# Performance work log

Hardware: AMD Instinct MI355X
Metric: run time of the kernel (lower is better)

## Reference

```python
import jax, jax.numpy as jnp
import numpy as np

N_NODES = 100000
N_EDGES = 2000000
FEAT = 4
H = 64
L = 3  # num_mp_layers
E = 2  # edge_types


def _p(key, shape, scale=0.05):
    return jax.random.normal(key, shape, dtype=jnp.float32) * scale


def setup_inputs() -> dict:
    key = jax.random.key(0)
    ks = jax.random.split(key, 24)
    inp = {
        "x": jax.random.normal(ks[0], (N_NODES, FEAT), dtype=jnp.float32),
        "node_type": jax.random.randint(ks[1], (N_NODES,), 0, 3),
        "edge_index": jax.random.randint(ks[2], (2, N_EDGES), 0, N_NODES),
        "edge_type": jax.random.randint(ks[3], (N_EDGES,), 0, E),
        # input_proj: Linear(4,64) + LayerNorm(64)
        "in_w": _p(ks[4], (FEAT, H)), "in_b": _p(ks[5], (H,)),
        "ln_g": jnp.ones((H,), jnp.float32), "ln_b": jnp.zeros((H,), jnp.float32),
        # per-layer, per-edge-type message MLPs: Linear(2H,H) -> ReLU -> Linear(H,H)
        "mlp_w1": _p(ks[6], (L, E, 2 * H, H)), "mlp_b1": _p(ks[7], (L, E, H)),
        "mlp_w2": _p(ks[8], (L, E, H, H)), "mlp_b2": _p(ks[9], (L, E, H)),
        # per-layer GRUCell(H,H): gates ordered [r, z, n] as in torch
        "gru_wi": _p(ks[10], (L, H, 3 * H)), "gru_wh": _p(ks[11], (L, H, 3 * H)),
        "gru_bi": _p(ks[12], (L, 3 * H)), "gru_bh": _p(ks[13], (L, 3 * H)),
        # readout: Linear(H,H) -> ReLU -> Linear(H,1)
        "ro_w1": _p(ks[14], (H, H)), "ro_b1": _p(ks[15], (H,)),
        "ro_w2": _p(ks[16], (H, 1)), "ro_b2": _p(ks[17], (1,)),
    }
    return inp


def _layernorm(h, g, b, eps=1e-5):
    mu = jnp.mean(h, axis=-1, keepdims=True)
    var = jnp.mean(jnp.square(h - mu), axis=-1, keepdims=True)
    return (h - mu) * jax.lax.rsqrt(var + eps) * g + b


def _forward(x, edge_index, edge_type, node_type,
             in_w, in_b, ln_g, ln_b,
             mlp_w1, mlp_b1, mlp_w2, mlp_b2,
             gru_wi, gru_wh, gru_bi, gru_bh,
             ro_w1, ro_b1, ro_w2, ro_b2):
    n = x.shape[0]
    # input projection (dropout is identity at inference)
    h = jax.nn.relu(_layernorm(x @ in_w + in_b, ln_g, ln_b))
    src, dst = edge_index[0], edge_index[1]
    for l in range(L):
        # gather -> concat: (M, 2H)
        mi = jnp.concatenate([h[src], h[dst]], axis=1)
        msg = jnp.zeros((mi.shape[0], H), dtype=h.dtype)
        for e in range(E):
            m = jax.nn.relu(mi @ mlp_w1[l, e] + mlp_b1[l, e]) @ mlp_w2[l, e] + mlp_b2[l, e]
            msg = msg + jnp.where((edge_type == e)[:, None], m, jnp.zeros((), h.dtype))
        # scatter_add over destination nodes
        agg = jax.ops.segment_sum(msg, dst, num_segments=n)
        # GRUCell(agg, h), torch gate order [r, z, n]
        gi = agg @ gru_wi[l] + gru_bi[l]
        gh = h @ gru_wh[l] + gru_bh[l]
        i_r, i_z, i_n = jnp.split(gi, 3, axis=-1)
        h_r, h_z, h_n = jnp.split(gh, 3, axis=-1)
        r = jax.nn.sigmoid(i_r + h_r)
        z = jax.nn.sigmoid(i_z + h_z)
        nn_ = jnp.tanh(i_n + r * h_n)
        h = (1.0 - z) * nn_ + z * h
    out = jax.nn.relu(h @ ro_w1 + ro_b1) @ ro_w2 + ro_b2  # (N, 1)
    # additive correction for data qubits (node_type==0); other nodes zeroed
    corr = jnp.where(node_type == 0, x[:, 0] + out[:, 0], jnp.zeros((), x.dtype))
    return corr


def reference(x, node_type, edge_index, edge_type,
              in_w, in_b, ln_g, ln_b,
              mlp_w1, mlp_b1, mlp_w2, mlp_b2,
              gru_wi, gru_wh, gru_bi, gru_bh,
              ro_w1, ro_b1, ro_w2, ro_b2):
    return _forward(x, edge_index, edge_type, node_type,
                    in_w, in_b, ln_g, ln_b,
                    mlp_w1, mlp_b1, mlp_w2, mlp_b2,
                    gru_wi, gru_wh, gru_bi, gru_bh,
                    ro_w1, ro_b1, ro_w2, ro_b2)
```

## Files before the change

kernel.cpp:

```cpp
#include <hip/hip_runtime.h>

typedef unsigned int u32;
typedef unsigned short u16;
typedef unsigned long long u64;

using short8 = __attribute__((ext_vector_type(8))) short;
using f32x4  = __attribute__((ext_vector_type(4))) float;

__device__ __forceinline__ u32 f2bf(float f) {
    u32 u = __float_as_uint(f);
    return (u + 0x7fffu + ((u >> 16) & 1u)) >> 16;
}
__device__ __forceinline__ u32 pk(float a, float b) {
    return f2bf(a) | (f2bf(b) << 16);
}
__device__ __forceinline__ u32 f2bf_fast(float f) {
    return (__float_as_uint(f) + 0x8000u) >> 16;
}
__device__ __forceinline__ u32 pk_fast(float a, float b) {
    return f2bf_fast(a) | (f2bf_fast(b) << 16);
}
__device__ __forceinline__ float bflo(u32 u) { return __uint_as_float(u << 16); }
__device__ __forceinline__ float bfhi(u32 u) { return __uint_as_float(u & 0xffff0000u); }
__device__ __forceinline__ float bfu(u16 u) { return __uint_as_float(((u32)u) << 16); }

union U8 { u32 u[4]; short8 v; };

__global__ void k_input_proj(const float* __restrict__ x, const float* __restrict__ in_w,
                             const float* __restrict__ in_b, const float* __restrict__ ln_g,
                             const float* __restrict__ ln_b, u16* __restrict__ hbf, int n_nodes) {
    const int lane = threadIdx.x & 63;
    const int node = blockIdx.x * 4 + (threadIdx.x >> 6);
    if (node >= n_nodes) return;
    float acc = in_b[lane];
#pragma unroll
    for (int k = 0; k < 4; ++k) acc = fmaf(x[node * 4 + k], in_w[k * 64 + lane], acc);
    float s = acc;
#pragma unroll
    for (int off = 32; off > 0; off >>= 1) s += __shfl_xor(s, off);
    float mu = s * (1.f / 64.f);
    float d = acc - mu;
    float vs = d * d;
#pragma unroll
    for (int off = 32; off > 0; off >>= 1) vs += __shfl_xor(vs, off);
    float inv = rsqrtf(vs * (1.f / 64.f) + 1e-5f);
    float hv = fmaxf(d * inv * ln_g[lane] + ln_b[lane], 0.f);
    hbf[(size_t)node * 64 + lane] = (u16)f2bf(hv);
}

__global__ void k_hist(const int* __restrict__ dst, const int* __restrict__ ety,
                       int* __restrict__ cnt, int M, int N) {
    int i = blockIdx.x * 256 + threadIdx.x;
    if (i < M) atomicAdd(&cnt[(ety[i] & 1) * N + dst[i]], 1);
}

__global__ void k_scan1(int* __restrict__ data, int* __restrict__ part, int N) {
    __shared__ int s[1024];
    const int t = threadIdx.x;
    const int i = blockIdx.x * 1024 + t;
    int v = (i < N) ? data[i] : 0;
    s[t] = v;
    __syncthreads();
#pragma unroll
    for (int d = 1; d < 1024; d <<= 1) {
        int x = (t >= d) ? s[t - d] : 0;
        __syncthreads();
        s[t] += x;
        __syncthreads();
    }
    if (i < N) data[i] = s[t] - v;
    if (t == 1023) part[blockIdx.x] = s[1023];
}

__global__ void k_scan2(int* __restrict__ part, int nb) {
    const int l = threadIdx.x & 63;
    int base = 0;
    for (int s = 0; s < nb; s += 64) {
        int i = s + l;
        int orig = (i < nb) ? part[i] : 0;
        int x = orig;
#pragma unroll
        for (int off = 1; off < 64; off <<= 1) {
            int t = __shfl_up(x, off);
            if (l >= off) x += t;
        }
        if (i < nb) part[i] = base + x - orig;
        base += __shfl(x, 63);
    }
}

__global__ void k_scan3(int* __restrict__ data, const int* __restrict__ part, int N,
                        int saveIdx, int* __restrict__ slot) {
    int i = blockIdx.x * 1024 + threadIdx.x;
    if (i < N) {
        int v = data[i] + part[blockIdx.x];
        data[i] = v;
        if (i == saveIdx) slot[0] = v;
    }
}

__global__ void k_filldst(const int* __restrict__ off, int* __restrict__ dstP,
                          int NB, int N, int M) {
    int b = blockIdx.x * 256 + threadIdx.x;
    if (b >= NB) return;
    int s = off[b];
    int e = (b + 1 < NB) ? off[b + 1] : M;
    int d = (b >= N) ? b - N : b;
    for (int p = s; p < e; ++p) dstP[p] = d;
}

__global__ void k_scatter(const int* __restrict__ src, const int* __restrict__ dst,
                          const int* __restrict__ ety, int* __restrict__ cursor,
                          int* __restrict__ srcP, int M, int N, int nd8) {
    const int g = blockIdx.x & 7;
    const int nb = gridDim.x >> 3;
    const int bi = blockIdx.x >> 3;
    for (int e = bi * 256 + threadIdx.x; e < M; e += nb * 256) {
        int d = dst[e];
        if (d / nd8 == g) {
            int t = ety[e] & 1;
            int pos = atomicAdd(&cursor[t * N + d], 1);
            srcP[pos] = src[e] & 0x3FFFFFFF;
        }
    }
}

__global__ __launch_bounds__(256, 2) void k_edge_mlp(
    const u16* __restrict__ hbf, const int* __restrict__ srcP, const int* __restrict__ dstP,
    const int* __restrict__ t0p, const float* __restrict__ w1, const float* __restrict__ b1,
    const float* __restrict__ w2, const float* __restrict__ b2,
    float* __restrict__ agg, int M) {
    __shared__ u16 sHid[4][4608];
    __shared__ u16 sMsg[4][4864];

    const int tid = threadIdx.x;
    const int l = tid & 63, wv = tid >> 6;
    const int l15 = l & 15, quad = l >> 4;
    const f32x4 vz = {0.f, 0.f, 0.f, 0.f};

    const int T0 = *t0p;
    const int half = gridDim.x >> 1;
    const int ty = (blockIdx.x >= half) ? 1 : 0;
    const int bi = ty ? (int)blockIdx.x - half : (int)blockIdx.x;

    const int n_tiles = (M + 63) >> 6;
    const int tlo = ty ? (T0 >> 6) : 0;
    const int thi = ty ? n_tiles : ((T0 + 63) >> 6);
    const int lo = ty ? T0 : 0;
    const int hi = ty ? M : T0;
    const int range = thi - tlo;
    const int per = (range + half - 1) / half;
    const int c0 = tlo + bi * per;
    const int c1 = min(c0 + per, thi);

    short8 Bf1[4][4], Bf2[2][4];
    float b1r[4], b2r[4];
#pragma unroll
    for (int ni = 0; ni < 4; ++ni) {
        const int c = ni * 16 + l15;
        b1r[ni] = b1[ty * 64 + c];
        b2r[ni] = b2[ty * 64 + c];
#pragma unroll
        for (int s = 0; s < 4; ++s) {
            U8 tmp;
            const float* wp = w1 + (size_t)ty * 8192 + (size_t)(s * 32 + quad * 8) * 64 + c;
#pragma unroll
            for (int jp = 0; jp < 4; ++jp) tmp.u[jp] = pk(wp[(2 * jp) * 64], wp[(2 * jp + 1) * 64]);
            Bf1[s][ni] = tmp.v;
        }
#pragma unroll
        for (int s = 0; s < 2; ++s) {
            U8 tmp;
            const float* wp = w2 + (size_t)ty * 4096 + (size_t)(s * 32 + quad * 8) * 64 + c;
#pragma unroll
            for (int jp = 0; jp < 4; ++jp) tmp.u[jp] = pk(wp[(2 * jp) * 64], wp[(2 * jp + 1) * 64]);
            Bf2[s][ni] = tmp.v;
        }
    }

    u16* hid = sHid[wv];
    u16* msg = sMsg[wv];

    int t = c0 + wv;
    int mdr_c = -1;
    int rs[4], rd[4];
    short8 a1[4][4];
    if (t < c1) {
        int ec = min((t << 6) + l, M - 1);
        int ms = srcP[ec];
        mdr_c = dstP[ec];
#pragma unroll
        for (int mi = 0; mi < 4; ++mi) {
            rs[mi] = __shfl(ms, mi * 16 + l15);
            rd[mi] = __shfl(mdr_c, mi * 16 + l15);
        }
#pragma unroll
        for (int mi = 0; mi < 4; ++mi)
#pragma unroll
            for (int s = 0; s < 4; ++s) {
                const int row = (s < 2) ? rs[mi] : rd[mi];
                a1[mi][s] = *(const short8*)(hbf + (size_t)row * 64 + (s & 1) * 32 + quad * 8);
            }
    }

    for (; t < c1; t += 4) {
        const int base = t << 6;
        const int ecn = min(((t + 4) << 6) + l, M - 1);
        int msr_n = srcP[ecn];
        int mdr_n = dstP[ecn];

#pragma unroll
        for (int mi = 0; mi < 4; ++mi) {
            f32x4 acc[4] = {vz, vz, vz, vz};
#pragma unroll
            for (int s = 0; s < 4; ++s)
#pragma unroll
                for (int ni = 0; ni < 4; ++ni)
                    acc[ni] = __builtin_amdgcn_mfma_f32_16x16x32_bf16(a1[mi][s], Bf1[s][ni], acc[ni], 0, 0, 0);
#pragma unroll
            for (int ni = 0; ni < 4; ++ni) {
                const int c = ni * 16 + l15;
#pragma unroll
                for (int r = 0; r < 4; ++r) {
                    float hv = fmaxf(acc[ni][r] + b1r[ni], 0.f);
                    hid[(mi * 16 + quad * 4 + r) * 72 + c] = (u16)f2bf_fast(hv);
                }
            }
        }

#pragma unroll
        for (int mi = 0; mi < 4; ++mi) {
            rs[mi] = __shfl(msr_n, mi * 16 + l15);
            rd[mi] = __shfl(mdr_n, mi * 16 + l15);
        }
#pragma unroll
        for (int mi = 0; mi < 4; ++mi)
#pragma unroll
            for (int s = 0; s < 4; ++s) {
                const int row = (s < 2) ? rs[mi] : rd[mi];
                a1[mi][s] = *(const short8*)(hbf + (size_t)row * 64 + (s & 1) * 32 + quad * 8);
            }

#pragma unroll
        for (int mi = 0; mi < 4; ++mi) {
            short8 a2a = *(const short8*)(hid + (mi * 16 + l15) * 72 + quad * 8);
            short8 a2b = *(const short8*)(hid + (mi * 16 + l15) * 72 + 32 + quad * 8);
#pragma unroll
            for (int ni = 0; ni < 4; ++ni) {
                f32x4 tt = __builtin_amdgcn_mfma_f32_16x16x32_bf16(a2a, Bf2[0][ni], vz, 0, 0, 0);
                f32x4 m2 = __builtin_amdgcn_mfma_f32_16x16x32_bf16(a2b, Bf2[1][ni], tt, 0, 0, 0);
                const int c = ni * 16 + l15;
                const int e0 = mi * 16 + quad * 4;
                const float bb = b2r[ni];
                *(u32*)(msg + c * 76 + e0) = pk_fast(m2[0] + bb, m2[1] + bb);
                *(u32*)(msg + c * 76 + e0 + 2) = pk_fast(m2[2] + bb, m2[3] + bb);
            }
        }

        {
            int eg = base + l;
            int dvz = (eg >= lo && eg < hi) ? mdr_c : -1;
            int dprev = __shfl_up(dvz, 1);
            u64 mask = __ballot((l == 0) || (dvz != dprev));
            float a = 0.f;
#pragma unroll
            for (int i = 0; i < 64; i += 4) {
                uint2 pr = *(const uint2*)(msg + l * 76 + i);
                float v0 = bflo(pr.x), v1 = bfhi(pr.x), v2 = bflo(pr.y), v3 = bfhi(pr.y);
#define RR_STEP(ii, vv)                                                         \
                a += (vv);                                                      \
                if ((ii) == 63 || ((mask >> ((ii) + 1)) & 1ull)) {              \
                    int dd = __builtin_amdgcn_readlane(dvz, (ii));              \
                    if (dd >= 0) unsafeAtomicAdd(agg + (size_t)dd * 64 + l, a); \
                    a = 0.f;                                                    \
                }
                RR_STEP(i, v0)
                RR_STEP(i + 1, v1)
                RR_STEP(i + 2, v2)
                RR_STEP(i + 3, v3)
#undef RR_STEP
            }
        }
        mdr_c = mdr_n;
    }
}

__global__ __launch_bounds__(256, 2) void k_gru_gemm(
    float* __restrict__ agg, u16* __restrict__ hbf,
    const float* __restrict__ wi, const float* __restrict__ wh,
    const float* __restrict__ bi, const float* __restrict__ bh, int n_nodes) {
    extern __shared__ u16 smem[];
    u16* sRZ = smem;
    u16* sIN = smem + 128 * 136;
    u16* sHN = sIN + 64 * 72;
    u16* sTR = sHN + 64 * 72;

    const int tid = threadIdx.x;
    const int l = tid & 63, wv = tid >> 6;
    const int l15 = l & 15, quad = l >> 4;
    const f32x4 vz = {0.f, 0.f, 0.f, 0.f};

    for (int u = tid; u < 128 * 64; u += 256) {
        int c = u & 127, k0 = (u >> 7) * 2;
        float v0 = (k0 < 64) ? wi[k0 * 192 + c] : wh[(k0 - 64) * 192 + c];
        float v1 = (k0 < 64) ? wi[(k0 + 1) * 192 + c] : wh[(k0 + 1 - 64) * 192 + c];
        *(u32*)(sRZ + c * 136 + k0) = pk(v0, v1);
    }
    for (int u = tid; u < 64 * 32; u += 256) {
        int c = u & 63, k0 = (u >> 6) * 2;
        *(u32*)(sIN + c * 72 + k0) = pk(wi[k0 * 192 + 128 + c], wi[(k0 + 1) * 192 + 128 + c]);
        *(u32*)(sHN + c * 72 + k0) = pk(wh[k0 * 192 + 128 + c], wh[(k0 + 1) * 192 + 128 + c]);
    }
    float bR[4], bZ[4], bI[4], bH[4];
#pragma unroll
    for (int nt = 0; nt < 4; ++nt) {
        int j = nt * 16 + l15;
        bR[nt] = bi[j] + bh[j];
        bZ[nt] = bi[64 + j] + bh[64 + j];
        bI[nt] = bi[128 + j];
        bH[nt] = bh[128 + j];
    }
    __syncthreads();

    u16* tr = sTR + wv * (16 * 72);
    const f32x4 z4 = {0.f, 0.f, 0.f, 0.f};
    const int n_tiles = (n_nodes + 15) >> 4;
    const int g = blockIdx.x & 7, jb = blockIdx.x >> 3, nbg = gridDim.x >> 3;
    const int per8 = (n_tiles + 7) >> 3;
    const int glo = g * per8, ghi = min(glo + per8, n_tiles);
    for (int tile = glo + jb * 4 + wv; tile < ghi; tile += nbg * 4) {
        const int nb = tile << 4;
        const int arow = nb + l15;
        const int rowc = (arow < n_nodes) ? arow : (n_nodes - 1);
        short8 aA[2], aH[2];
#pragma unroll
        for (int s = 0; s < 2; ++s) {
            const float* ap = agg + (size_t)rowc * 64 + s * 32 + quad * 8;
            U8 tt;
#pragma unroll
            for (int jp = 0; jp < 4; ++jp) tt.u[jp] = pk(ap[2 * jp], ap[2 * jp + 1]);
            aA[s] = tt.v;
            aH[s] = *(const short8*)(hbf + (size_t)rowc * 64 + s * 32 + quad * 8);
        }
        if (arow < n_nodes) {
#pragma unroll
            for (int s = 0; s < 2; ++s) {
                *(f32x4*)(agg + (size_t)rowc * 64 + s * 32 + quad * 8) = z4;
                *(f32x4*)(agg + (size_t)rowc * 64 + s * 32 + quad * 8 + 4) = z4;
            }
        }
        f32x4 D[16];
#pragma unroll
        for (int i = 0; i < 16; ++i) D[i] = vz;
#pragma unroll
        for (int nt = 0; nt < 8; ++nt) {
            const u16* bp = sRZ + (nt * 16 + l15) * 136 + quad * 8;
            D[nt] = __builtin_amdgcn_mfma_f32_16x16x32_bf16(aA[0], *(const short8*)bp, D[nt], 0, 0, 0);
            D[nt] = __builtin_amdgcn_mfma_f32_16x16x32_bf16(aA[1], *(const short8*)(bp + 32), D[nt], 0, 0, 0);
            D[nt] = __builtin_amdgcn_mfma_f32_16x16x32_bf16(aH[0], *(const short8*)(bp + 64), D[nt], 0, 0, 0);
            D[nt] = __builtin_amdgcn_mfma_f32_16x16x32_bf16(aH[1], *(const short8*)(bp + 96), D[nt], 0, 0, 0);
        }
#pragma unroll
        for (int nt = 0; nt < 4; ++nt) {
            const u16* ip = sIN + (nt * 16 + l15) * 72 + quad * 8;
            D[8 + nt] = __builtin_amdgcn_mfma_f32_16x16x32_bf16(aA[0], *(const short8*)ip, D[8 + nt], 0, 0, 0);
            D[8 + nt] = __builtin_amdgcn_mfma_f32_16x16x32_bf16(aA[1], *(const short8*)(ip + 32), D[8 + nt], 0, 0, 0);
            const u16* hp = sHN + (nt * 16 + l15) * 72 + quad * 8;
            D[12 + nt] = __builtin_amdgcn_mfma_f32_16x16x32_bf16(aH[0], *(const short8*)hp, D[12 + nt], 0, 0, 0);
            D[12 + nt] = __builtin_amdgcn_mfma_f32_16x16x32_bf16(aH[1], *(const short8*)(hp + 32), D[12 + nt], 0, 0, 0);
        }
#pragma unroll
        for (int nt = 0; nt < 4; ++nt) {
            const int j = nt * 16 + l15;
#pragma unroll
            for (int r = 0; r < 4; ++r) {
                const int nd = nb + quad * 4 + r;
                float rsv = D[nt][r] + bR[nt];
                float zsv = D[4 + nt][r] + bZ[nt];
                float inv = D[8 + nt][r] + bI[nt];
                float hnv = D[12 + nt][r] + bH[nt];
                float rr = 1.f / (1.f + __expf(-rsv));
                float zz = 1.f / (1.f + __expf(-zsv));
                float nn = tanhf(fmaf(rr, hnv, inv));
                float hv = (nd < n_nodes) ? bfu(hbf[(size_t)nd * 64 + j]) : 0.f;
                float nh = (1.f - zz) * nn + zz * hv;
                tr[(quad * 4 + r) * 72 + j] = (u16)f2bf(nh);
            }
        }
        {
            const int nd = nb + (l >> 2);
            if (nd < n_nodes) {
                const u16* sp = tr + (l >> 2) * 72 + (l & 3) * 16;
                uint4 va = *(const uint4*)sp;
                uint4 vb = *(const uint4*)(sp + 8);
                u16* dp = hbf + (size_t)nd * 64 + (l & 3) * 16;
                *(uint4*)dp = va;
                *(uint4*)(dp + 8) = vb;
            }
        }
    }
}

__global__ void k_readout(const u16* __restrict__ hbf, const float* __restrict__ x,
                          const int* __restrict__ node_type, const float* __restrict__ w1,
                          const float* __restrict__ b1, const float* __restrict__ w2,
                          const float* __restrict__ b2, float* __restrict__ out, int n_nodes) {
    const int lane = threadIdx.x & 63;
    const int node = blockIdx.x * 4 + (threadIdx.x >> 6);
    if (node >= n_nodes) return;
    float hv = bfu(hbf[(size_t)node * 64 + lane]);
    float acc = b1[lane];
    for (int k = 0; k < 64; ++k) acc = fmaf(__shfl(hv, k), w1[k * 64 + lane], acc);
    float t = fmaxf(acc, 0.f) * w2[lane];
#pragma unroll
    for (int off = 32; off > 0; off >>= 1) t += __shfl_xor(t, off);
    if (lane == 0) {
        float o = t + b2[0];
        out[node] = (node_type[node] == 0) ? (x[node * 4] + o) : 0.f;
    }
}

extern "C" void kernel_launch(void* const* d_in, const int* in_sizes, int n_in, void* d_out,
                              int out_size, void* d_ws, size_t ws_size, hipStream_t stream) {
    const float* x = (const float*)d_in[0];
    const int* node_type = (const int*)d_in[1];
    const int* edge_index = (const int*)d_in[2];
    const int* edge_type = (const int*)d_in[3];
    const float* in_w = (const float*)d_in[4];
    const float* in_b = (const float*)d_in[5];
    const float* ln_g = (const float*)d_in[6];
    const float* ln_b = (const float*)d_in[7];
    const float* mlp_w1 = (const float*)d_in[8];
    const float* mlp_b1 = (const float*)d_in[9];
    const float* mlp_w2 = (const float*)d_in[10];
    const float* mlp_b2 = (const float*)d_in[11];
    const float* gru_wi = (const float*)d_in[12];
    const float* gru_wh = (const float*)d_in[13];
    const float* gru_bi = (const float*)d_in[14];
    const float* gru_bh = (const float*)d_in[15];
    const float* ro_w1 = (const float*)d_in[16];
    const float* ro_b1 = (const float*)d_in[17];
    const float* ro_w2 = (const float*)d_in[18];
    const float* ro_b2 = (const float*)d_in[19];

    const int N = in_sizes[1];
    const int M = in_sizes[3];
    const int* src = edge_index;
    const int* dst = edge_index + M;

    char* wsb = (char*)d_ws;
    float* agg = (float*)wsb;
    u16* hbf = (u16*)(wsb + (size_t)N * 256);
    int* off = (int*)(wsb + (size_t)N * 384);
    int* part = (int*)(wsb + (size_t)N * 384 + (size_t)2 * N * 4);
    int* srcP = (int*)(wsb + (size_t)N * 384 + (size_t)2 * N * 4 + 4096);
    int* dstP = srcP + M;
    int* t0slot = part + 1000;

    const int NB = 2 * N;
    const int nb = (NB + 1023) / 1024;
    const int nd8 = (N + 7) / 8;

    hipMemsetAsync(off, 0, (size_t)NB * sizeof(int), stream);
    k_hist<<<(M + 255) / 256, 256, 0, stream>>>(dst, edge_type, off, M, N);
    k_scan1<<<nb, 1024, 0, stream>>>(off, part, NB);
    k_scan2<<<1, 64, 0, stream>>>(part, nb);
    k_scan3<<<nb, 1024, 0, stream>>>(off, part, NB, N, t0slot);
    k_filldst<<<(NB + 255) / 256, 256, 0, stream>>>(off, dstP, NB, N, M);
    k_scatter<<<2048, 256, 0, stream>>>(src, dst, edge_type, off, srcP, M, N, nd8);

    k_input_proj<<<(N + 3) / 4, 256, 0, stream>>>(x, in_w, in_b, ln_g, ln_b, hbf, N);
    hipMemsetAsync(agg, 0, (size_t)N * 64 * sizeof(float), stream);
    const size_t gruLds = (size_t)(128 * 136 + 64 * 72 + 64 * 72 + 4 * 16 * 72) * sizeof(u16);
    for (int l = 0; l < 3; ++l) {
        k_edge_mlp<<<1024, 256, 0, stream>>>(hbf, srcP, dstP, t0slot,
                                             mlp_w1 + (size_t)l * 2 * 128 * 64,
                                             mlp_b1 + (size_t)l * 2 * 64,
                                             mlp_w2 + (size_t)l * 2 * 64 * 64,
                                             mlp_b2 + (size_t)l * 2 * 64, agg, M);
        k_gru_gemm<<<1024, 256, gruLds, stream>>>(agg, hbf, gru_wi + (size_t)l * 64 * 192,
                                                  gru_wh + (size_t)l * 64 * 192,
                                                  gru_bi + (size_t)l * 192, gru_bh + (size_t)l * 192, N);
    }
    k_readout<<<(N + 3) / 4, 256, 0, stream>>>(hbf, x, node_type, ro_w1, ro_b1, ro_w2, ro_b2,
                                               (float*)d_out, N);
}
```

Measured before the change: 835.9 us.

## Deepen edge index prefetch and interleave gather loads with first MLP GEMM

Edge src/dst indices are now prefetched two tiles ahead instead of one, so index loads have a full iteration to land before they feed the h-row gathers. The next tile's row gathers are issued per row-block right after that block's first-layer MFMAs, spreading memory traffic across the compute instead of bunching it after the GEMM. The two 32-bit message stores to LDS are merged into one 64-bit store. The price is extra live registers for the deeper prefetch, which may hurt occupancy or cause spills.

After: 824.7 us. About the same (-1.3%).

```diff
diff --git a/kernel.cpp b/kernel.cpp
--- a/kernel.cpp
+++ b/kernel.cpp
@@ -182,32 +182,33 @@
     u16* msg = sMsg[wv];
 
     int t = c0 + wv;
-    int mdr_c = -1;
-    int rs[4], rd[4];
+    int mdc = -1;
+    int msn = 0, mdn = -1;
     short8 a1[4][4];
     if (t < c1) {
         int ec = min((t << 6) + l, M - 1);
         int ms = srcP[ec];
-        mdr_c = dstP[ec];
+        mdc = dstP[ec];
 #pragma unroll
         for (int mi = 0; mi < 4; ++mi) {
-            rs[mi] = __shfl(ms, mi * 16 + l15);
-            rd[mi] = __shfl(mdr_c, mi * 16 + l15);
-        }
-#pragma unroll
-        for (int mi = 0; mi < 4; ++mi)
+            int rs = __shfl(ms, mi * 16 + l15);
+            int rd = __shfl(mdc, mi * 16 + l15);
 #pragma unroll
             for (int s = 0; s < 4; ++s) {
-                const int row = (s < 2) ? rs[mi] : rd[mi];
+                const int row = (s < 2) ? rs : rd;
                 a1[mi][s] = *(const short8*)(hbf + (size_t)row * 64 + (s & 1) * 32 + quad * 8);
             }
+        }
+        int ecn = min(((t + 4) << 6) + l, M - 1);
+        msn = srcP[ecn];
+        mdn = dstP[ecn];
     }
 
     for (; t < c1; t += 4) {
         const int base = t << 6;
-        const int ecn = min(((t + 4) << 6) + l, M - 1);
-        int msr_n = srcP[ecn];
-        int mdr_n = dstP[ecn];
+        const int ecf = min(((t + 8) << 6) + l, M - 1);
+        const int msf = srcP[ecf];
+        const int mdf = dstP[ecf];
 
 #pragma unroll
         for (int mi = 0; mi < 4; ++mi) {
@@ -217,6 +218,15 @@
 #pragma unroll
                 for (int ni = 0; ni < 4; ++ni)
                     acc[ni] = __builtin_amdgcn_mfma_f32_16x16x32_bf16(a1[mi][s], Bf1[s][ni], acc[ni], 0, 0, 0);
+            {
+                int rs = __shfl(msn, mi * 16 + l15);
+                int rd = __shfl(mdn, mi * 16 + l15);
+#pragma unroll
+                for (int s = 0; s < 4; ++s) {
+                    const int row = (s < 2) ? rs : rd;
+                    a1[mi][s] = *(const short8*)(hbf + (size_t)row * 64 + (s & 1) * 32 + quad * 8);
+                }
+            }
 #pragma unroll
             for (int ni = 0; ni < 4; ++ni) {
                 const int c = ni * 16 + l15;
@@ -227,19 +237,6 @@
                 }
             }
         }
-
-#pragma unroll
-        for (int mi = 0; mi < 4; ++mi) {
-            rs[mi] = __shfl(msr_n, mi * 16 + l15);
-            rd[mi] = __shfl(mdr_n, mi * 16 + l15);
-        }
-#pragma unroll
-        for (int mi = 0; mi < 4; ++mi)
-#pragma unroll
-            for (int s = 0; s < 4; ++s) {
-                const int row = (s < 2) ? rs[mi] : rd[mi];
-                a1[mi][s] = *(const short8*)(hbf + (size_t)row * 64 + (s & 1) * 32 + quad * 8);
-            }
 
 #pragma unroll
         for (int mi = 0; mi < 4; ++mi) {
@@ -252,14 +249,16 @@
                 const int c = ni * 16 + l15;
                 const int e0 = mi * 16 + quad * 4;
                 const float bb = b2r[ni];
-                *(u32*)(msg + c * 76 + e0) = pk_fast(m2[0] + bb, m2[1] + bb);
-                *(u32*)(msg + c * 76 + e0 + 2) = pk_fast(m2[2] + bb, m2[3] + bb);
+                uint2 w;
+                w.x = pk_fast(m2[0] + bb, m2[1] + bb);
+                w.y = pk_fast(m2[2] + bb, m2[3] + bb);
+                *(uint2*)(msg + c * 76 + e0) = w;
             }
         }
 
         {
             int eg = base + l;
-            int dvz = (eg >= lo && eg < hi) ? mdr_c : -1;
+            int dvz = (eg >= lo && eg < hi) ? mdc : -1;
             int dprev = __shfl_up(dvz, 1);
             u64 mask = __ballot((l == 0) || (dvz != dprev));
             float a = 0.f;
@@ -281,7 +280,9 @@
 #undef RR_STEP
             }
         }
-        mdr_c = mdr_n;
+        mdc = mdn;
+        msn = msf;
+        mdn = mdf;
     }
 }
 
```
